# Kernel tuning notes

Hardware: AMD Instinct MI355X
Metric: run time of the kernel (lower is better)

## Reference

```python
import jax, jax.numpy as jnp
import numpy as np

B, C, H, G, NCLS = 32, 256, 128, 128, 2  # graphs, nodes-per-graph==in_channels, hidden, matrix pool, classes
N = B * C                                # total nodes = 8192
E = 131072


def setup_inputs() -> dict:
    key = jax.random.key(0)
    ks = jax.random.split(key, 12)
    gain = 5.0 / 3.0
    xav = gain * np.sqrt(6.0 / (C + C))  # xavier_uniform bound for [C,C]
    return {
        "x": jax.random.normal(ks[0], (N, C), jnp.float32),
        "edge_index": jax.random.randint(ks[1], (2, E), 0, N),
        "graph_id": jax.random.randint(ks[2], (B,), 0, G),
        "batch": jnp.arange(N) // C,
        "pert_W": jax.random.uniform(ks[3], (G, C, C), jnp.float32, -xav, xav),
        "pert_b": jax.random.uniform(ks[4], (G, C, C), jnp.float32, -xav, xav),
        "mask_W": jax.random.uniform(ks[5], (G, C, C), jnp.float32, -xav, xav),
        "gcn_w0": jax.random.normal(ks[6], (C, H), jnp.float32) / np.sqrt(C),
        "gcn_w1": jax.random.normal(ks[7], (H, H), jnp.float32) / np.sqrt(H),
        "gcn_w2": jax.random.normal(ks[8], (H, H), jnp.float32) / np.sqrt(H),
        "mlp_W": jax.random.normal(ks[9], (2 * H, NCLS), jnp.float32) / np.sqrt(2 * H),
        "mlp_b": jnp.zeros((NCLS,), jnp.float32),
    }


def _hard_where(s):
    # MyWhere: 0 if s <= 0.5 else 1
    return jnp.where(s <= 0.5, 0.0, 1.0).astype(s.dtype)


def _predictor(x, adj, batch, gcn_w0, gcn_w1, gcn_w2, mlp_W, mlp_b):
    # GCN encoder: h <- relu(A @ h @ W); readout = concat(mean-pool, max-pool); MLP+sigmoid
    h = x
    for W in (gcn_w0, gcn_w1, gcn_w2):
        h = jax.nn.relu(adj @ (h @ W))
    sums = jax.ops.segment_sum(h, batch, num_segments=B)
    cnt = jax.ops.segment_sum(jnp.ones((h.shape[0], 1), h.dtype), batch, num_segments=B)
    mean = sums / jnp.maximum(cnt, 1.0)
    mx = jax.ops.segment_max(h, batch, num_segments=B)
    pooled = jnp.concatenate([mean, mx], axis=-1)  # [B, 2H]
    return jax.nn.sigmoid(pooled @ mlp_W + mlp_b)


def reference(x, edge_index, graph_id, batch, pert_W, pert_b, mask_W,
              gcn_w0, gcn_w1, gcn_w2, mlp_W, mlp_b):
    # dense adjacency (duplicate edges sum, matching sparse_coo.to_dense)
    adj = jnp.zeros((N, N), jnp.float32).at[edge_index[0], edge_index[1]].add(1.0)
    P = pert_W[graph_id]    # [B, C, C] block-diag blocks
    bias = pert_b[graph_id]  # [B, C, C] block-diag bias blocks
    # block_diag(P) @ adj == per-block GEMM over row stripes
    PA = jnp.einsum('bij,bjn->bin', P, adj.reshape(B, C, N))  # [B, C, N]
    PA = PA.reshape(B, C, B, C).at[jnp.arange(B), :, jnp.arange(B), :].add(bias)
    PA = PA.reshape(N, N)
    pert_adj = _hard_where(jax.nn.sigmoid(PA))
    M = _hard_where(jax.nn.sigmoid(mask_W[graph_id].reshape(N, C)))
    x_masked = M * x
    pred = _predictor(x, adj, batch, gcn_w0, gcn_w1, gcn_w2, mlp_W, mlp_b)
    aug_pred = _predictor(x_masked, pert_adj, batch, gcn_w0, gcn_w1, gcn_w2, mlp_W, mlp_b)
    return (adj, pert_adj, M, pred, aug_pred, x_masked)
```

## Files before the change

### kernel.cpp

```cpp
#include <hip/hip_runtime.h>
#include <hip/hip_bf16.h>

#define NN 8192
#define CC 256
#define BBg 32
#define HH 128
#define EE 131072

typedef __attribute__((ext_vector_type(8))) short short8;
typedef __attribute__((ext_vector_type(4))) float f32x4;
typedef unsigned long long ull;

__device__ __forceinline__ float hard01(float v) {
    if (v >= 1e-6f) return 1.0f;
    if (v <= 0.0f) return 0.0f;
    float ef = (float)exp(-(double)v);
    float s = 1.0f / (1.0f + ef);
    return (s > 0.5f) ? 1.0f : 0.0f;
}

__device__ __forceinline__ unsigned short f2bf(float f) {
    unsigned u = __float_as_uint(f);
    u += 0x7FFFu + ((u >> 16) & 1u);
    return (unsigned short)(u >> 16);
}
__device__ __forceinline__ float bf2f(unsigned short b) {
    return __uint_as_float(((unsigned)b) << 16);
}

__global__ void k_hist(const int* __restrict__ ei, int* __restrict__ rowcnt,
                       int* __restrict__ colcnt, unsigned char* __restrict__ coljs) {
    int e = blockIdx.x * 256 + threadIdx.x;
    if (e >= EE) return;
    int r = ei[e], c = ei[EE + e];
    atomicAdd(&rowcnt[r], 1);
    int idx = (r >> 8) * NN + c;
    int slot = atomicAdd(&colcnt[idx], 1);
    if (slot < 16) coljs[(size_t)idx * 16 + slot] = (unsigned char)(r & 255);
}

__global__ void k_scan(const int* __restrict__ rowcnt, int* __restrict__ rowptr,
                       int* __restrict__ rowfill) {
    __shared__ int sums[256];
    int t = threadIdx.x;
    int base = t * 32;
    int loc[32];
    int s = 0;
    #pragma unroll
    for (int i = 0; i < 32; ++i) { loc[i] = s; s += rowcnt[base + i]; }
    sums[t] = s;
    __syncthreads();
    if (t == 0) {
        int a = 0;
        for (int i = 0; i < 256; ++i) { int v = sums[i]; sums[i] = a; a += v; }
        rowptr[NN] = a;
    }
    __syncthreads();
    int off = sums[t];
    #pragma unroll
    for (int i = 0; i < 32; ++i) {
        rowptr[base + i] = off + loc[i];
        rowfill[base + i] = off + loc[i];
    }
}

__global__ void k_fill(const int* __restrict__ ei, int* __restrict__ rowfill,
                       int* __restrict__ csrcol) {
    int e = blockIdx.x * 256 + threadIdx.x;
    if (e >= EE) return;
    int r = ei[e], c = ei[EE + e];
    int pos = atomicAdd(&rowfill[r], 1);
    csrcol[pos] = c;
}

__global__ void __launch_bounds__(256) k_adj_write(const int* __restrict__ rowptr,
                                                   const int* __restrict__ csrcol,
                                                   float* __restrict__ adj) {
    __shared__ int cnt[NN];
    int row = blockIdx.x, t = threadIdx.x;
    int4 z = make_int4(0, 0, 0, 0);
    #pragma unroll
    for (int i = 0; i < 8; ++i) *(int4*)&cnt[(i * 256 + t) * 4] = z;
    __syncthreads();
    int start = rowptr[row], end = rowptr[row + 1];
    for (int e = start + t; e < end; e += 256) atomicAdd(&cnt[csrcol[e]], 1);
    __syncthreads();
    float* dst = adj + (size_t)row * NN;
    #pragma unroll
    for (int i = 0; i < 8; ++i) {
        int p = i * 1024 + t * 4;
        float4 f;
        f.x = (float)cnt[p + 0]; f.y = (float)cnt[p + 1];
        f.z = (float)cnt[p + 2]; f.w = (float)cnt[p + 3];
        *(float4*)(dst + p) = f;
    }
}

__global__ void k_mask(const float* __restrict__ maskW, const int* __restrict__ gid,
                       const float* __restrict__ x, float* __restrict__ Mo,
                       float* __restrict__ xm) {
    int i = blockIdx.x * 256 + threadIdx.x;
    int base = i * 4;
    int r = base >> 8;
    int c = base & 255;
    int g = gid[r >> 8];
    float4 mv = *(const float4*)(maskW + ((size_t)g << 16) + ((size_t)(r & 255) << 8) + c);
    float4 xv = *(const float4*)(x + ((size_t)r << 8) + c);
    float4 m, o;
    m.x = hard01(mv.x); m.y = hard01(mv.y); m.z = hard01(mv.z); m.w = hard01(mv.w);
    o.x = m.x * xv.x; o.y = m.y * xv.y; o.z = m.z * xv.z; o.w = m.w * xv.w;
    *(float4*)(Mo + ((size_t)r << 8) + c) = m;
    *(float4*)(xm + ((size_t)r << 8) + c) = o;
}

__global__ void __launch_bounds__(256) k_pertadj(const float* __restrict__ pertW,
                                                 const float* __restrict__ pertB,
                                                 const int* __restrict__ gid,
                                                 const int* __restrict__ colcnt,
                                                 const unsigned char* __restrict__ coljs,
                                                 float* __restrict__ padj,
                                                 unsigned char* __restrict__ padjbits) {
    __shared__ float Pl[32][257];
    int nc = blockIdx.x & 3, rt = (blockIdx.x >> 2) & 7, b = blockIdx.x >> 5;
    int t = threadIdx.x;
    int g = gid[b];
    const float* src = pertW + ((size_t)g << 16) + (size_t)rt * 32 * CC;
    #pragma unroll 4
    for (int i = 0; i < 32; ++i) Pl[i][t] = src[i * CC + t];
    __syncthreads();
    int ty = t >> 6, tx = t & 63;
    int ro = ty * 8;
    const float* bsrc = pertB + ((size_t)g << 16) + (size_t)(rt * 32 + ro) * CC;
    for (int it = 0; it < 4; ++it) {
        int n0 = nc * 2048 + it * 512 + tx * 8;
        float s[8][8];
        #pragma unroll
        for (int ii = 0; ii < 8; ++ii)
            #pragma unroll
            for (int cc = 0; cc < 8; ++cc) s[ii][cc] = 0.0f;
        #pragma unroll
        for (int half = 0; half < 2; ++half) {
            int n = n0 + half * 4;
            int cidx = b * NN + n;
            int4 cnt4 = *(const int4*)(colcnt + cidx);
            const uint4* jp = (const uint4*)(coljs + (size_t)cidx * 16);
            #pragma unroll
            for (int cc = 0; cc < 4; ++cc) {
                int cnt = (&cnt4.x)[cc];
                cnt = cnt > 16 ? 16 : cnt;
                if (cnt == 0) continue;
                uint4 jv = jp[cc];
                for (int q = 0; q < cnt; ++q) {
                    unsigned word = (q < 8) ? ((q < 4) ? jv.x : jv.y)
                                            : ((q < 12) ? jv.z : jv.w);
                    int j = (word >> ((q & 3) * 8)) & 255;
                    #pragma unroll
                    for (int ii = 0; ii < 8; ++ii) s[ii][half * 4 + cc] += Pl[ro + ii][j];
                }
            }
        }
        bool diag = ((n0 >> 8) == b);
        #pragma unroll
        for (int ii = 0; ii < 8; ++ii) {
            if (diag) {
                const float* bp = bsrc + (size_t)ii * CC + (n0 & 255);
                #pragma unroll
                for (int cc = 0; cc < 8; ++cc) s[ii][cc] += bp[cc];
            }
            float f[8];
            unsigned byte = 0;
            #pragma unroll
            for (int cc = 0; cc < 8; ++cc) {
                f[cc] = hard01(s[ii][cc]);
                if (f[cc] != 0.f) byte |= (1u << cc);
            }
            size_t ob = (size_t)(b * CC + rt * 32 + ro + ii) * NN + n0;
            float4 f0, f1;
            f0.x = f[0]; f0.y = f[1]; f0.z = f[2]; f0.w = f[3];
            f1.x = f[4]; f1.y = f[5]; f1.z = f[6]; f1.w = f[7];
            *(float4*)(padj + ob) = f0;
            *(float4*)(padj + ob + 4) = f1;
            size_t bb = (size_t)(b * CC + rt * 32 + ro + ii) * (NN / 8)
                        + nc * 256 + it * 64 + tx;
            padjbits[bb] = (unsigned char)byte;
        }
    }
}

__global__ void __launch_bounds__(256) k_gemm_dual(const float* __restrict__ Ap,
                                                   const float* __restrict__ Aa,
                                                   const float* __restrict__ W,
                                                   float* __restrict__ Zp,
                                                   unsigned short* __restrict__ Zthi,
                                                   unsigned short* __restrict__ Ztlo,
                                                   int K, int relu, int aparts, int apstride) {
    __shared__ float Alp[32][68];
    __shared__ float Ala[32][68];
    __shared__ float Wl[64][132];
    int mt = blockIdx.x;
    int t = threadIdx.x;
    int ty = t >> 3, tx = t & 7;
    float accp[16], acca[16];
    #pragma unroll
    for (int u = 0; u < 16; ++u) { accp[u] = 0.0f; acca[u] = 0.0f; }
    for (int kc = 0; kc < K; kc += 64) {
        int row = t >> 3, q = t & 7;
        {
            const float* ap = Ap + (size_t)(mt * 32 + row) * K + kc + q * 8;
            float4 f0 = *(const float4*)ap;
            float4 f1 = *(const float4*)(ap + 4);
            if (relu) {
                f0.x = fmaxf(f0.x, 0.f); f0.y = fmaxf(f0.y, 0.f);
                f0.z = fmaxf(f0.z, 0.f); f0.w = fmaxf(f0.w, 0.f);
                f1.x = fmaxf(f1.x, 0.f); f1.y = fmaxf(f1.y, 0.f);
                f1.z = fmaxf(f1.z, 0.f); f1.w = fmaxf(f1.w, 0.f);
            }
            *(float4*)&Alp[row][q * 8] = f0;
            *(float4*)&Alp[row][q * 8 + 4] = f1;
        }
        {
            const float* ap = Aa + (size_t)(mt * 32 + row) * K + kc + q * 8;
            float4 f0 = *(const float4*)ap;
            float4 f1 = *(const float4*)(ap + 4);
            for (int p = 1; p < aparts; ++p) {
                float4 g0 = *(const float4*)(ap + (size_t)p * apstride);
                float4 g1 = *(const float4*)(ap + (size_t)p * apstride + 4);
                f0.x += g0.x; f0.y += g0.y; f0.z += g0.z; f0.w += g0.w;
                f1.x += g1.x; f1.y += g1.y; f1.z += g1.z; f1.w += g1.w;
            }
            if (relu) {
                f0.x = fmaxf(f0.x, 0.f); f0.y = fmaxf(f0.y, 0.f);
                f0.z = fmaxf(f0.z, 0.f); f0.w = fmaxf(f0.w, 0.f);
                f1.x = fmaxf(f1.x, 0.f); f1.y = fmaxf(f1.y, 0.f);
                f1.z = fmaxf(f1.z, 0.f); f1.w = fmaxf(f1.w, 0.f);
            }
            *(float4*)&Ala[row][q * 8] = f0;
            *(float4*)&Ala[row][q * 8 + 4] = f1;
        }
        {
            int wrow = t >> 2, wq = t & 3;
            const float* wp = W + (size_t)(kc + wrow) * HH + wq * 32;
            #pragma unroll
            for (int u = 0; u < 32; u += 4)
                *(float4*)&Wl[wrow][wq * 32 + u] = *(const float4*)(wp + u);
        }
        __syncthreads();
        #pragma unroll 2
        for (int kk = 0; kk < 64; ++kk) {
            float a = Alp[ty][kk];
            float b2 = Ala[ty][kk];
            #pragma unroll
            for (int u = 0; u < 16; u += 4) {
                float4 wv = *(const float4*)(&Wl[kk][tx * 16 + u]);
                accp[u + 0] += a * wv.x; accp[u + 1] += a * wv.y;
                accp[u + 2] += a * wv.z; accp[u + 3] += a * wv.w;
                acca[u + 0] += b2 * wv.x; acca[u + 1] += b2 * wv.y;
                acca[u + 2] += b2 * wv.z; acca[u + 3] += b2 * wv.w;
            }
        }
        __syncthreads();
    }
    {
        float* cp = Zp + (size_t)(mt * 32 + ty) * HH + tx * 16;
        #pragma unroll
        for (int u = 0; u < 16; u += 4) {
            float4 f;
            f.x = accp[u]; f.y = accp[u + 1]; f.z = accp[u + 2]; f.w = accp[u + 3];
            *(float4*)(cp + u) = f;
        }
    }
    {
        __syncthreads();
        float* Tl = &Wl[0][0];
        #pragma unroll
        for (int u = 0; u < 16; ++u) Tl[ty * 132 + tx * 16 + u] = acca[u];
        __syncthreads();
        int col = t >> 1, half = t & 1;
        unsigned short hu[16] __attribute__((aligned(16)));
        unsigned short lu[16] __attribute__((aligned(16)));
        #pragma unroll
        for (int rr = 0; rr < 16; ++rr) {
            float v = Tl[(half * 16 + rr) * 132 + col];
            unsigned short hb = f2bf(v);
            hu[rr] = hb;
            lu[rr] = f2bf(v - bf2f(hb));
        }
        size_t ob = (size_t)col * NN + mt * 32 + half * 16;
        *(uint4*)(Zthi + ob)     = *(const uint4*)&hu[0];
        *(uint4*)(Zthi + ob + 8) = *(const uint4*)&hu[8];
        *(uint4*)(Ztlo + ob)     = *(const uint4*)&lu[0];
        *(uint4*)(Ztlo + ob + 8) = *(const uint4*)&lu[8];
    }
}

__global__ void k_spmm_gather(const int* __restrict__ rowptr,
                              const int* __restrict__ csrcol,
                              const float* __restrict__ Z,
                              float* __restrict__ S) {
    int t = threadIdx.x;
    int row = blockIdx.x * 2 + (t >> 7);
    int col = t & 127;
    int start = rowptr[row], end = rowptr[row + 1];
    float s0 = 0.f, s1 = 0.f;
    int e = start;
    for (; e + 2 <= end; e += 2) {
        int c0 = csrcol[e], c1 = csrcol[e + 1];
        s0 += Z[(size_t)c0 * HH + col];
        s1 += Z[(size_t)c1 * HH + col];
    }
    if (e < end) s0 += Z[(size_t)csrcol[e] * HH + col];
    S[(size_t)row * HH + col] = s0 + s1;
}

__global__ void __launch_bounds__(256) k_mfma_spmm(const unsigned char* __restrict__ padjbits,
                                                   const unsigned short* __restrict__ Zthi,
                                                   const unsigned short* __restrict__ Ztlo,
                                                   float* __restrict__ Sp) {
    __shared__ unsigned short Bh[2][128 * 40];
    __shared__ unsigned short Bl[2][128 * 40];
    int mt = blockIdx.x >> 3, sk = blockIdx.x & 7;
    int t = threadIdx.x, w = t >> 6, lane = t & 63;
    int quad = lane >> 4, l15 = lane & 15;
    f32x4 acc[4][8];
    #pragma unroll
    for (int m = 0; m < 4; ++m)
        #pragma unroll
        for (int i = 0; i < 8; ++i) acc[m][i] = (f32x4){0.f, 0.f, 0.f, 0.f};
    int bn = t >> 1, bq = t & 1;
    const unsigned short* zh = Zthi + (size_t)bn * NN + sk * 1024 + bq * 16;
    const unsigned short* zl = Ztlo + (size_t)bn * NN + sk * 1024 + bq * 16;
    int row0 = mt * 256 + w * 64 + l15;
    const unsigned* ab[4];
    #pragma unroll
    for (int m = 0; m < 4; ++m)
        ab[m] = (const unsigned*)(padjbits + (size_t)(row0 + m * 16) * (NN / 8)) + sk * 32;
    int ldsw = bn * 40 + bq * 16;
    int bmb = l15 * 40 + quad * 8;
    uint4 rh0, rh1, rl0, rl1;
    unsigned bits[4], nbits[4];
    rh0 = *(const uint4*)(zh + 0);
    rh1 = *(const uint4*)(zh + 8);
    rl0 = *(const uint4*)(zl + 0);
    rl1 = *(const uint4*)(zl + 8);
    #pragma unroll
    for (int m = 0; m < 4; ++m) bits[m] = ab[m][0];
    *(uint4*)(&Bh[0][ldsw + 0]) = rh0;
    *(uint4*)(&Bh[0][ldsw + 8]) = rh1;
    *(uint4*)(&Bl[0][ldsw + 0]) = rl0;
    *(uint4*)(&Bl[0][ldsw + 8]) = rl1;
    __syncthreads();
    for (int st = 0; st < 32; ++st) {
        int cur = st & 1;
        if (st < 31) {
            int k = (st + 1) * 32;
            rh0 = *(const uint4*)(zh + k);
            rh1 = *(const uint4*)(zh + k + 8);
            rl0 = *(const uint4*)(zl + k);
            rl1 = *(const uint4*)(zl + k + 8);
            #pragma unroll
            for (int m = 0; m < 4; ++m) nbits[m] = ab[m][st + 1];
        }
        short8 a[4];
        #pragma unroll
        for (int m = 0; m < 4; ++m) {
            unsigned byte = (bits[m] >> (quad * 8)) & 0xFFu;
            #pragma unroll
            for (int j = 0; j < 8; ++j)
                a[m][j] = (byte & (1u << j)) ? (short)0x3F80 : (short)0;
        }
        #pragma unroll
        for (int nt = 0; nt < 8; ++nt) {
            short8 fh = *(const short8*)(&Bh[cur][nt * 16 * 40 + bmb]);
            short8 fl = *(const short8*)(&Bl[cur][nt * 16 * 40 + bmb]);
            #pragma unroll
            for (int m = 0; m < 4; ++m) {
                acc[m][nt] = __builtin_amdgcn_mfma_f32_16x16x32_bf16(a[m], fh, acc[m][nt], 0, 0, 0);
                acc[m][nt] = __builtin_amdgcn_mfma_f32_16x16x32_bf16(a[m], fl, acc[m][nt], 0, 0, 0);
            }
        }
        if (st < 31) {
            *(uint4*)(&Bh[1 - cur][ldsw + 0]) = rh0;
            *(uint4*)(&Bh[1 - cur][ldsw + 8]) = rh1;
            *(uint4*)(&Bl[1 - cur][ldsw + 0]) = rl0;
            *(uint4*)(&Bl[1 - cur][ldsw + 8]) = rl1;
            #pragma unroll
            for (int m = 0; m < 4; ++m) bits[m] = nbits[m];
        }
        __syncthreads();
    }
    int dc = l15, dr = quad * 4;
    float* base = Sp + (size_t)sk * NN * HH + (size_t)(mt * 256 + w * 64 + dr) * HH;
    #pragma unroll
    for (int m = 0; m < 4; ++m)
        #pragma unroll
        for (int nt = 0; nt < 8; ++nt)
            #pragma unroll
            for (int r = 0; r < 4; ++r)
                base[(size_t)(m * 16 + r) * HH + nt * 16 + dc] = acc[m][nt][r];
}

__global__ void __launch_bounds__(256) k_pool2(const float* __restrict__ S,
                                               const float* __restrict__ Sp,
                                               const float* __restrict__ mlpW,
                                               const float* __restrict__ mlpb,
                                               float* __restrict__ pred,
                                               float* __restrict__ augp,
                                               int apstride) {
    __shared__ float ps[256], pm[256], pl[256], r0[256], r1[256];
    int aug = blockIdx.x >> 5, g = blockIdx.x & 31, t = threadIdx.x;
    const float* Sb = aug ? Sp : S;
    int parts = aug ? 8 : 1;
    float* outp = aug ? augp : pred;
    int col = t & 127, half = t >> 7;
    const float* base = Sb + (size_t)(g * CC + half * 128) * HH + col;
    float sum = 0.f, mx = -3.0e38f;
    for (int rr = 0; rr < 128; ++rr) {
        float v = base[(size_t)rr * HH];
        for (int p = 1; p < parts; ++p) v += base[(size_t)p * apstride + (size_t)rr * HH];
        v = fmaxf(v, 0.f);
        sum += v;
        mx = fmaxf(mx, v);
    }
    ps[t] = sum; pm[t] = mx;
    __syncthreads();
    if (half == 0) {
        pl[col] = (ps[col] + ps[col + 128]) * (1.0f / 256.0f);
        pl[col + 128] = fmaxf(pm[col], pm[col + 128]);
    }
    __syncthreads();
    r0[t] = pl[t] * mlpW[t * 2 + 0];
    r1[t] = pl[t] * mlpW[t * 2 + 1];
    __syncthreads();
    for (int sft = 128; sft > 0; sft >>= 1) {
        if (t < sft) { r0[t] += r0[t + sft]; r1[t] += r1[t + sft]; }
        __syncthreads();
    }
    if (t == 0) {
        float l0 = r0[0] + mlpb[0];
        float l1 = r1[0] + mlpb[1];
        outp[g * 2 + 0] = 1.0f / (1.0f + expf(-l0));
        outp[g * 2 + 1] = 1.0f / (1.0f + expf(-l1));
    }
}

extern "C" void kernel_launch(void* const* d_in, const int* in_sizes, int n_in,
                              void* d_out, int out_size, void* d_ws, size_t ws_size,
                              hipStream_t stream) {
    (void)in_sizes; (void)n_in; (void)out_size; (void)ws_size;
    const float* x     = (const float*)d_in[0];
    const int*   ei    = (const int*)d_in[1];
    const int*   gid   = (const int*)d_in[2];
    const float* pertW = (const float*)d_in[4];
    const float* pertB = (const float*)d_in[5];
    const float* maskW = (const float*)d_in[6];
    const float* w0    = (const float*)d_in[7];
    const float* w1    = (const float*)d_in[8];
    const float* w2    = (const float*)d_in[9];
    const float* mlpW  = (const float*)d_in[10];
    const float* mlpb  = (const float*)d_in[11];

    float* out  = (float*)d_out;
    float* adj  = out;
    float* padj = out + (size_t)NN * NN;
    float* Mo   = out + 2 * (size_t)NN * NN;
    float* pred = Mo + (size_t)NN * CC;
    float* augp = pred + (size_t)BBg * 2;
    float* xm   = augp + (size_t)BBg * 2;

    char* ws = (char*)d_ws;
    int*            colcnt   = (int*)ws;
    int*            rowcnt   = (int*)(ws + (1 << 20));
    int*            rowptr   = (int*)(ws + (1 << 20) + (64 << 10));
    int*            rowfill  = (int*)(ws + (1 << 20) + (128 << 10));
    unsigned char*  coljs    = (unsigned char*)(ws + (2 << 20));
    int*            csrcol   = (int*)(ws + (6 << 20));
    float*          Z        = (float*)(ws + (7 << 20));
    float*          S        = (float*)(ws + (11 << 20));
    unsigned short* Zthi     = (unsigned short*)(ws + (15 << 20));
    unsigned short* Ztlo     = (unsigned short*)(ws + (17 << 20));
    float*          Sp       = (float*)(ws + (19 << 20));
    unsigned char*  padjbits = (unsigned char*)(ws + (51 << 20));
    const int PS = NN * HH;

    hipMemsetAsync(colcnt, 0, (1 << 20) + (32 << 10), stream);
    k_hist<<<EE / 256, 256, 0, stream>>>(ei, rowcnt, colcnt, coljs);
    k_scan<<<1, 256, 0, stream>>>(rowcnt, rowptr, rowfill);
    k_fill<<<EE / 256, 256, 0, stream>>>(ei, rowfill, csrcol);
    k_adj_write<<<NN, 256, 0, stream>>>(rowptr, csrcol, adj);
    k_mask<<<(NN * CC / 4) / 256, 256, 0, stream>>>(maskW, gid, x, Mo, xm);
    k_pertadj<<<1024, 256, 0, stream>>>(pertW, pertB, gid, colcnt, coljs, padj, padjbits);

    k_gemm_dual<<<256, 256, 0, stream>>>(x, xm, w0, Z, Zthi, Ztlo, 256, 0, 1, 0);
    k_spmm_gather<<<NN / 2, 256, 0, stream>>>(rowptr, csrcol, Z, S);
    k_mfma_spmm<<<256, 256, 0, stream>>>(padjbits, Zthi, Ztlo, Sp);
    k_gemm_dual<<<256, 256, 0, stream>>>(S, Sp, w1, Z, Zthi, Ztlo, 128, 1, 8, PS);
    k_spmm_gather<<<NN / 2, 256, 0, stream>>>(rowptr, csrcol, Z, S);
    k_mfma_spmm<<<256, 256, 0, stream>>>(padjbits, Zthi, Ztlo, Sp);
    k_gemm_dual<<<256, 256, 0, stream>>>(S, Sp, w2, Z, Zthi, Ztlo, 128, 1, 8, PS);
    k_spmm_gather<<<NN / 2, 256, 0, stream>>>(rowptr, csrcol, Z, S);
    k_mfma_spmm<<<256, 256, 0, stream>>>(padjbits, Zthi, Ztlo, Sp);
    k_pool2<<<64, 256, 0, stream>>>(S, Sp, mlpW, mlpb, pred, augp, PS);
}
```

Baseline: 1.064 ms.

## Merge independent stages into shared launches via block-index dispatch

Independent kernels are packed into combined launches that branch on block index. Histogram runs with masking, scan with the perturbed-adjacency build, CSR fill with the first dense GEMM, and the dense adjacency write with the first MFMA SpMM. This removes several launches and lets independent work overlap on the GPU. In exchange, blocks of unequal cost share a grid, and the MFMA kernel's shared-memory footprint now also applies to the adjacency-write blocks.

```diff
diff --git a/kernel.cpp b/kernel.cpp
--- a/kernel.cpp
+++ b/kernel.cpp
@@ -28,101 +28,69 @@
     return __uint_as_float(((unsigned)b) << 16);
 }
 
-__global__ void k_hist(const int* __restrict__ ei, int* __restrict__ rowcnt,
-                       int* __restrict__ colcnt, unsigned char* __restrict__ coljs) {
-    int e = blockIdx.x * 256 + threadIdx.x;
-    if (e >= EE) return;
-    int r = ei[e], c = ei[EE + e];
-    atomicAdd(&rowcnt[r], 1);
-    int idx = (r >> 8) * NN + c;
-    int slot = atomicAdd(&colcnt[idx], 1);
-    if (slot < 16) coljs[(size_t)idx * 16 + slot] = (unsigned char)(r & 255);
-}
-
-__global__ void k_scan(const int* __restrict__ rowcnt, int* __restrict__ rowptr,
-                       int* __restrict__ rowfill) {
+__global__ void k_hist_mask(const int* __restrict__ ei, int* __restrict__ rowcnt,
+                            int* __restrict__ colcnt, unsigned char* __restrict__ coljs,
+                            const float* __restrict__ maskW, const int* __restrict__ gid,
+                            const float* __restrict__ x, float* __restrict__ Mo,
+                            float* __restrict__ xm) {
+    int blk = blockIdx.x, t = threadIdx.x;
+    if (blk < 512) {
+        int e = blk * 256 + t;
+        int r = ei[e], c = ei[EE + e];
+        atomicAdd(&rowcnt[r], 1);
+        int idx = (r >> 8) * NN + c;
+        int slot = atomicAdd(&colcnt[idx], 1);
+        if (slot < 16) coljs[(size_t)idx * 16 + slot] = (unsigned char)(r & 255);
+    } else {
+        int i = (blk - 512) * 256 + t;
+        int base = i * 4;
+        int r = base >> 8;
+        int c = base & 255;
+        int g = gid[r >> 8];
+        float4 mv = *(const float4*)(maskW + ((size_t)g << 16) + ((size_t)(r & 255) << 8) + c);
+        float4 xv = *(const float4*)(x + ((size_t)r << 8) + c);
+        float4 m, o;
+        m.x = hard01(mv.x); m.y = hard01(mv.y); m.z = hard01(mv.z); m.w = hard01(mv.w);
+        o.x = m.x * xv.x; o.y = m.y * xv.y; o.z = m.z * xv.z; o.w = m.w * xv.w;
+        *(float4*)(Mo + ((size_t)r << 8) + c) = m;
+        *(float4*)(xm + ((size_t)r << 8) + c) = o;
+    }
+}
+
+__global__ void __launch_bounds__(256) k_scan_pertadj(
+        const int* __restrict__ rowcnt, int* __restrict__ rowptr,
+        int* __restrict__ rowfill,
+        const float* __restrict__ pertW, const float* __restrict__ pertB,
+        const int* __restrict__ gid, const int* __restrict__ colcnt,
+        const unsigned char* __restrict__ coljs,
+        float* __restrict__ padj, unsigned char* __restrict__ padjbits) {
+    __shared__ float Pl[32][257];
     __shared__ int sums[256];
     int t = threadIdx.x;
-    int base = t * 32;
-    int loc[32];
-    int s = 0;
-    #pragma unroll
-    for (int i = 0; i < 32; ++i) { loc[i] = s; s += rowcnt[base + i]; }
-    sums[t] = s;
-    __syncthreads();
-    if (t == 0) {
-        int a = 0;
-        for (int i = 0; i < 256; ++i) { int v = sums[i]; sums[i] = a; a += v; }
-        rowptr[NN] = a;
-    }
-    __syncthreads();
-    int off = sums[t];
-    #pragma unroll
-    for (int i = 0; i < 32; ++i) {
-        rowptr[base + i] = off + loc[i];
-        rowfill[base + i] = off + loc[i];
-    }
-}
-
-__global__ void k_fill(const int* __restrict__ ei, int* __restrict__ rowfill,
-                       int* __restrict__ csrcol) {
-    int e = blockIdx.x * 256 + threadIdx.x;
-    if (e >= EE) return;
-    int r = ei[e], c = ei[EE + e];
-    int pos = atomicAdd(&rowfill[r], 1);
-    csrcol[pos] = c;
-}
-
-__global__ void __launch_bounds__(256) k_adj_write(const int* __restrict__ rowptr,
-                                                   const int* __restrict__ csrcol,
-                                                   float* __restrict__ adj) {
-    __shared__ int cnt[NN];
-    int row = blockIdx.x, t = threadIdx.x;
-    int4 z = make_int4(0, 0, 0, 0);
-    #pragma unroll
-    for (int i = 0; i < 8; ++i) *(int4*)&cnt[(i * 256 + t) * 4] = z;
-    __syncthreads();
-    int start = rowptr[row], end = rowptr[row + 1];
-    for (int e = start + t; e < end; e += 256) atomicAdd(&cnt[csrcol[e]], 1);
-    __syncthreads();
-    float* dst = adj + (size_t)row * NN;
-    #pragma unroll
-    for (int i = 0; i < 8; ++i) {
-        int p = i * 1024 + t * 4;
-        float4 f;
-        f.x = (float)cnt[p + 0]; f.y = (float)cnt[p + 1];
-        f.z = (float)cnt[p + 2]; f.w = (float)cnt[p + 3];
-        *(float4*)(dst + p) = f;
-    }
-}
-
-__global__ void k_mask(const float* __restrict__ maskW, const int* __restrict__ gid,
-                       const float* __restrict__ x, float* __restrict__ Mo,
-                       float* __restrict__ xm) {
-    int i = blockIdx.x * 256 + threadIdx.x;
-    int base = i * 4;
-    int r = base >> 8;
-    int c = base & 255;
-    int g = gid[r >> 8];
-    float4 mv = *(const float4*)(maskW + ((size_t)g << 16) + ((size_t)(r & 255) << 8) + c);
-    float4 xv = *(const float4*)(x + ((size_t)r << 8) + c);
-    float4 m, o;
-    m.x = hard01(mv.x); m.y = hard01(mv.y); m.z = hard01(mv.z); m.w = hard01(mv.w);
-    o.x = m.x * xv.x; o.y = m.y * xv.y; o.z = m.z * xv.z; o.w = m.w * xv.w;
-    *(float4*)(Mo + ((size_t)r << 8) + c) = m;
-    *(float4*)(xm + ((size_t)r << 8) + c) = o;
-}
-
-__global__ void __launch_bounds__(256) k_pertadj(const float* __restrict__ pertW,
-                                                 const float* __restrict__ pertB,
-                                                 const int* __restrict__ gid,
-                                                 const int* __restrict__ colcnt,
-                                                 const unsigned char* __restrict__ coljs,
-                                                 float* __restrict__ padj,
-                                                 unsigned char* __restrict__ padjbits) {
-    __shared__ float Pl[32][257];
-    int nc = blockIdx.x & 3, rt = (blockIdx.x >> 2) & 7, b = blockIdx.x >> 5;
-    int t = threadIdx.x;
+    if (blockIdx.x == 0) {
+        int base = t * 32;
+        int loc[32];
+        int s = 0;
+        #pragma unroll
+        for (int i = 0; i < 32; ++i) { loc[i] = s; s += rowcnt[base + i]; }
+        sums[t] = s;
+        __syncthreads();
+        if (t == 0) {
+            int a = 0;
+            for (int i = 0; i < 256; ++i) { int v = sums[i]; sums[i] = a; a += v; }
+            rowptr[NN] = a;
+        }
+        __syncthreads();
+        int off = sums[t];
+        #pragma unroll
+        for (int i = 0; i < 32; ++i) {
+            rowptr[base + i] = off + loc[i];
+            rowfill[base + i] = off + loc[i];
+        }
+        return;
+    }
+    int bid = blockIdx.x - 1;
+    int nc = bid & 3, rt = (bid >> 2) & 7, b = bid >> 5;
     int g = gid[b];
     const float* src = pertW + ((size_t)g << 16) + (size_t)rt * 32 * CC;
     #pragma unroll 4
@@ -187,18 +155,13 @@
     }
 }
 
-__global__ void __launch_bounds__(256) k_gemm_dual(const float* __restrict__ Ap,
-                                                   const float* __restrict__ Aa,
-                                                   const float* __restrict__ W,
-                                                   float* __restrict__ Zp,
-                                                   unsigned short* __restrict__ Zthi,
-                                                   unsigned short* __restrict__ Ztlo,
-                                                   int K, int relu, int aparts, int apstride) {
-    __shared__ float Alp[32][68];
-    __shared__ float Ala[32][68];
-    __shared__ float Wl[64][132];
-    int mt = blockIdx.x;
-    int t = threadIdx.x;
+__device__ __forceinline__ void gemm_dual_body(
+        int mt, int t,
+        const float* __restrict__ Ap, const float* __restrict__ Aa,
+        const float* __restrict__ W, float* __restrict__ Zp,
+        unsigned short* __restrict__ Zthi, unsigned short* __restrict__ Ztlo,
+        int K, int relu, int aparts, int apstride,
+        float (*Alp)[68], float (*Ala)[68], float (*Wl)[132]) {
     int ty = t >> 3, tx = t & 7;
     float accp[16], acca[16];
     #pragma unroll
@@ -293,33 +256,48 @@
     }
 }
 
-__global__ void k_spmm_gather(const int* __restrict__ rowptr,
-                              const int* __restrict__ csrcol,
-                              const float* __restrict__ Z,
-                              float* __restrict__ S) {
-    int t = threadIdx.x;
-    int row = blockIdx.x * 2 + (t >> 7);
-    int col = t & 127;
-    int start = rowptr[row], end = rowptr[row + 1];
-    float s0 = 0.f, s1 = 0.f;
-    int e = start;
-    for (; e + 2 <= end; e += 2) {
-        int c0 = csrcol[e], c1 = csrcol[e + 1];
-        s0 += Z[(size_t)c0 * HH + col];
-        s1 += Z[(size_t)c1 * HH + col];
-    }
-    if (e < end) s0 += Z[(size_t)csrcol[e] * HH + col];
-    S[(size_t)row * HH + col] = s0 + s1;
-}
-
-__global__ void __launch_bounds__(256) k_mfma_spmm(const unsigned char* __restrict__ padjbits,
-                                                   const unsigned short* __restrict__ Zthi,
-                                                   const unsigned short* __restrict__ Ztlo,
-                                                   float* __restrict__ Sp) {
-    __shared__ unsigned short Bh[2][128 * 40];
-    __shared__ unsigned short Bl[2][128 * 40];
-    int mt = blockIdx.x >> 3, sk = blockIdx.x & 7;
-    int t = threadIdx.x, w = t >> 6, lane = t & 63;
+__global__ void __launch_bounds__(256) k_gemm_fill(
+        const float* __restrict__ Ap, const float* __restrict__ Aa,
+        const float* __restrict__ W, float* __restrict__ Zp,
+        unsigned short* __restrict__ Zthi, unsigned short* __restrict__ Ztlo,
+        int K, int relu, int aparts, int apstride,
+        const int* __restrict__ ei, int* __restrict__ rowfill,
+        int* __restrict__ csrcol) {
+    __shared__ float Alp[32][68];
+    __shared__ float Ala[32][68];
+    __shared__ float Wl[64][132];
+    int blk = blockIdx.x, t = threadIdx.x;
+    if (blk < 256) {
+        gemm_dual_body(blk, t, Ap, Aa, W, Zp, Zthi, Ztlo, K, relu, aparts, apstride,
+                       Alp, Ala, Wl);
+    } else {
+        int e = (blk - 256) * 256 + t;
+        int r = ei[e], c = ei[EE + e];
+        int pos = atomicAdd(&rowfill[r], 1);
+        csrcol[pos] = c;
+    }
+}
+
+__global__ void __launch_bounds__(256) k_gemm_dual(
+        const float* __restrict__ Ap, const float* __restrict__ Aa,
+        const float* __restrict__ W, float* __restrict__ Zp,
+        unsigned short* __restrict__ Zthi, unsigned short* __restrict__ Ztlo,
+        int K, int relu, int aparts, int apstride) {
+    __shared__ float Alp[32][68];
+    __shared__ float Ala[32][68];
+    __shared__ float Wl[64][132];
+    gemm_dual_body(blockIdx.x, threadIdx.x, Ap, Aa, W, Zp, Zthi, Ztlo,
+                   K, relu, aparts, apstride, Alp, Ala, Wl);
+}
+
+__device__ __forceinline__ void mfma_body(
+        int blk, int t,
+        const unsigned char* __restrict__ padjbits,
+        const unsigned short* __restrict__ Zthi,
+        const unsigned short* __restrict__ Ztlo,
+        float* __restrict__ Sp, unsigned short* BhBase, unsigned short* BlBase) {
+    int mt = blk >> 3, sk = blk & 7;
+    int w = t >> 6, lane = t & 63;
     int quad = lane >> 4, l15 = lane & 15;
     f32x4 acc[4][8];
     #pragma unroll
@@ -344,10 +322,10 @@
     rl1 = *(const uint4*)(zl + 8);
     #pragma unroll
     for (int m = 0; m < 4; ++m) bits[m] = ab[m][0];
-    *(uint4*)(&Bh[0][ldsw + 0]) = rh0;
-    *(uint4*)(&Bh[0][ldsw + 8]) = rh1;
-    *(uint4*)(&Bl[0][ldsw + 0]) = rl0;
-    *(uint4*)(&Bl[0][ldsw + 8]) = rl1;
+    *(uint4*)(BhBase + ldsw + 0) = rh0;
+    *(uint4*)(BhBase + ldsw + 8) = rh1;
+    *(uint4*)(BlBase + ldsw + 0) = rl0;
+    *(uint4*)(BlBase + ldsw + 8) = rl1;
     __syncthreads();
     for (int st = 0; st < 32; ++st) {
         int cur = st & 1;
@@ -368,10 +346,12 @@
             for (int j = 0; j < 8; ++j)
                 a[m][j] = (byte & (1u << j)) ? (short)0x3F80 : (short)0;
         }
+        const unsigned short* Bh = BhBase + cur * 5120;
+        const unsigned short* Bl = BlBase + cur * 5120;
         #pragma unroll
         for (int nt = 0; nt < 8; ++nt) {
-            short8 fh = *(const short8*)(&Bh[cur][nt * 16 * 40 + bmb]);
-            short8 fl = *(const short8*)(&Bl[cur][nt * 16 * 40 + bmb]);
+            short8 fh = *(const short8*)(Bh + nt * 16 * 40 + bmb);
+            short8 fl = *(const short8*)(Bl + nt * 16 * 40 + bmb);
             #pragma unroll
             for (int m = 0; m < 4; ++m) {
                 acc[m][nt] = __builtin_amdgcn_mfma_f32_16x16x32_bf16(a[m], fh, acc[m][nt], 0, 0, 0);
@@ -379,10 +359,12 @@
             }
         }
         if (st < 31) {
-            *(uint4*)(&Bh[1 - cur][ldsw + 0]) = rh0;
-            *(uint4*)(&Bh[1 - cur][ldsw + 8]) = rh1;
-            *(uint4*)(&Bl[1 - cur][ldsw + 0]) = rl0;
-            *(uint4*)(&Bl[1 - cur][ldsw + 8]) = rl1;
+            unsigned short* BhN = BhBase + (1 - cur) * 5120;
+            unsigned short* BlN = BlBase + (1 - cur) * 5120;
+            *(uint4*)(BhN + ldsw + 0) = rh0;
+            *(uint4*)(BhN + ldsw + 8) = rh1;
+            *(uint4*)(BlN + ldsw + 0) = rl0;
+            *(uint4*)(BlN + ldsw + 8) = rl1;
             #pragma unroll
             for (int m = 0; m < 4; ++m) bits[m] = nbits[m];
         }
@@ -397,6 +379,69 @@
             #pragma unroll
             for (int r = 0; r < 4; ++r)
                 base[(size_t)(m * 16 + r) * HH + nt * 16 + dc] = acc[m][nt][r];
+}
+
+__global__ void __launch_bounds__(256) k_mfma_adj(
+        const unsigned char* __restrict__ padjbits,
+        const unsigned short* __restrict__ Zthi,
+        const unsigned short* __restrict__ Ztlo,
+        float* __restrict__ Sp,
+        const int* __restrict__ rowptr, const int* __restrict__ csrcol,
+        float* __restrict__ adj) {
+    __shared__ __align__(16) char smem[40960];
+    int blk = blockIdx.x, t = threadIdx.x;
+    if (blk < 256) {
+        mfma_body(blk, t, padjbits, Zthi, Ztlo, Sp,
+                  (unsigned short*)smem, (unsigned short*)(smem + 20480));
+    } else {
+        int* cnt = (int*)smem;
+        int row = blk - 256;
+        int4 z = make_int4(0, 0, 0, 0);
+        #pragma unroll
+        for (int i = 0; i < 8; ++i) *(int4*)&cnt[(i * 256 + t) * 4] = z;
+        __syncthreads();
+        int start = rowptr[row], end = rowptr[row + 1];
+        for (int e = start + t; e < end; e += 256) atomicAdd(&cnt[csrcol[e]], 1);
+        __syncthreads();
+        float* dst = adj + (size_t)row * NN;
+        #pragma unroll
+        for (int i = 0; i < 8; ++i) {
+            int p = i * 1024 + t * 4;
+            float4 f;
+            f.x = (float)cnt[p + 0]; f.y = (float)cnt[p + 1];
+            f.z = (float)cnt[p + 2]; f.w = (float)cnt[p + 3];
+            *(float4*)(dst + p) = f;
+        }
+    }
+}
+
+__global__ void __launch_bounds__(256) k_mfma_spmm(
+        const unsigned char* __restrict__ padjbits,
+        const unsigned short* __restrict__ Zthi,
+        const unsigned short* __restrict__ Ztlo,
+        float* __restrict__ Sp) {
+    __shared__ __align__(16) char smem[40960];
+    mfma_body(blockIdx.x, threadIdx.x, padjbits, Zthi, Ztlo, Sp,
+              (unsigned short*)smem, (unsigned short*)(smem + 20480));
+}
+
+__global__ void k_spmm_gather(const int* __restrict__ rowptr,
+                              const int* __restrict__ csrcol,
+                              const float* __restrict__ Z,
+                              float* __restrict__ S) {
+    int t = threadIdx.x;
+    int row = blockIdx.x * 2 + (t >> 7);
+    int col = t & 127;
+    int start = rowptr[row], end = rowptr[row + 1];
+    float s0 = 0.f, s1 = 0.f;
+    int e = start;
+    for (; e + 2 <= end; e += 2) {
+        int c0 = csrcol[e], c1 = csrcol[e + 1];
+        s0 += Z[(size_t)c0 * HH + col];
+        s1 += Z[(size_t)c1 * HH + col];
+    }
+    if (e < end) s0 += Z[(size_t)csrcol[e] * HH + col];
+    S[(size_t)row * HH + col] = s0 + s1;
 }
 
 __global__ void __launch_bounds__(256) k_pool2(const float* __restrict__ S,
@@ -483,16 +528,16 @@
     const int PS = NN * HH;
 
     hipMemsetAsync(colcnt, 0, (1 << 20) + (32 << 10), stream);
-    k_hist<<<EE / 256, 256, 0, stream>>>(ei, rowcnt, colcnt, coljs);
-    k_scan<<<1, 256, 0, stream>>>(rowcnt, rowptr, rowfill);
-    k_fill<<<EE / 256, 256, 0, stream>>>(ei, rowfill, csrcol);
-    k_adj_write<<<NN, 256, 0, stream>>>(rowptr, csrcol, adj);
-    k_mask<<<(NN * CC / 4) / 256, 256, 0, stream>>>(maskW, gid, x, Mo, xm);
-    k_pertadj<<<1024, 256, 0, stream>>>(pertW, pertB, gid, colcnt, coljs, padj, padjbits);
-
-    k_gemm_dual<<<256, 256, 0, stream>>>(x, xm, w0, Z, Zthi, Ztlo, 256, 0, 1, 0);
+    k_hist_mask<<<2560, 256, 0, stream>>>(ei, rowcnt, colcnt, coljs,
+                                          maskW, gid, x, Mo, xm);
+    k_scan_pertadj<<<1025, 256, 0, stream>>>(rowcnt, rowptr, rowfill,
+                                             pertW, pertB, gid, colcnt, coljs,
+                                             padj, padjbits);
+    k_gemm_fill<<<768, 256, 0, stream>>>(x, xm, w0, Z, Zthi, Ztlo, 256, 0, 1, 0,
+                                         ei, rowfill, csrcol);
+    k_mfma_adj<<<256 + NN, 256, 0, stream>>>(padjbits, Zthi, Ztlo, Sp,
+                                             rowptr, csrcol, adj);
     k_spmm_gather<<<NN / 2, 256, 0, stream>>>(rowptr, csrcol, Z, S);
-    k_mfma_spmm<<<256, 256, 0, stream>>>(padjbits, Zthi, Ztlo, Sp);
     k_gemm_dual<<<256, 256, 0, stream>>>(S, Sp, w1, Z, Zthi, Ztlo, 128, 1, 8, PS);
     k_spmm_gather<<<NN / 2, 256, 0, stream>>>(rowptr, csrcol, Z, S);
     k_mfma_spmm<<<256, 256, 0, stream>>>(padjbits, Zthi, Ztlo, Sp);
```

After: 998.6 us. 1.07x faster.
